# Performance work log

Hardware: AMD Instinct MI355X
Metric: run time of the kernel (lower is better)

Reference implementation:

```python
import jax, jax.numpy as jnp
import numpy as np

N_NODES = 100000
N_EDGES = 600000
N_GRAPHS = 8
D_IN = 256
H = 128
N_CONV = 2  # layers [128,128,128] -> first_h + 2 GINConvs
BN_EPS = 1e-5


def _bn_eval(x, p):
    # p: [4, H] rows = (gamma, beta, running_mean, running_var); eval-mode BatchNorm1d
    g, b, m, v = p[0], p[1], p[2], p[3]
    return (x - m) * jax.lax.rsqrt(v + BN_EPS) * g + b


def setup_inputs() -> dict:
    key = jax.random.key(0)
    ks = jax.random.split(key, 12)
    x = jax.random.normal(ks[0], (N_NODES, D_IN), dtype=jnp.float32)
    edge_index = jax.random.randint(ks[1], (2, N_EDGES), 0, N_NODES, dtype=jnp.int64 if jax.config.jax_enable_x64 else jnp.int32)
    batch = jnp.sort(jax.random.randint(ks[2], (N_NODES,), 0, N_GRAPHS))
    s = 0.05
    w_first = jax.random.normal(ks[3], (D_IN, H), dtype=jnp.float32) * s
    b_first = jax.random.normal(ks[4], (H,), dtype=jnp.float32) * s

    def bn_params(k):
        k1, k2, k3, k4 = jax.random.split(k, 4)
        gamma = jax.random.uniform(k1, (H,), minval=0.5, maxval=1.5)
        beta = jax.random.normal(k2, (H,)) * 0.1
        mean = jax.random.normal(k3, (H,)) * 0.1
        var = jax.random.uniform(k4, (H,), minval=0.5, maxval=1.5)
        return jnp.stack([gamma, beta, mean, var])  # [4, H]

    bn_first = bn_params(ks[5])
    w_conv = jax.random.normal(ks[6], (N_CONV, H, H), dtype=jnp.float32) * s
    b_conv = jax.random.normal(ks[7], (N_CONV, H), dtype=jnp.float32) * s
    bn_conv = jnp.stack([bn_params(k) for k in jax.random.split(ks[8], N_CONV)])  # [2,4,H]
    w_lin = jax.random.normal(ks[9], (N_CONV + 1, H, 1), dtype=jnp.float32) * s
    b_lin = jax.random.normal(ks[10], (N_CONV + 1, 1), dtype=jnp.float32) * s
    return {"x": x, "edge_index": edge_index, "batch": batch,
            "w_first": w_first, "b_first": b_first, "bn_first": bn_first,
            "w_conv": w_conv, "b_conv": b_conv, "bn_conv": bn_conv,
            "w_lin": w_lin, "b_lin": b_lin}


def reference(x, edge_index, batch, w_first, b_first, bn_first, w_conv, b_conv, bn_conv, w_lin, b_lin):
    src, dst = edge_index[0], edge_index[1]
    # first_h: Linear + BN(eval) + ReLU
    h = jax.nn.relu(_bn_eval(x @ w_first + b_first, bn_first))  # [N, H]

    # layer 0: node-level linear head + global max pool
    node_pred = h @ w_lin[0] + b_lin[0]  # [N, 1]
    wsi_pred = jax.ops.segment_max(node_pred, batch, num_segments=N_GRAPHS)  # [G, 1]

    for l in range(N_CONV):
        # GINConv (eps=0, sum aggregation): nn((1+eps)*x_i + sum_{j->i} x_j)
        agg = jax.ops.segment_sum(h[src], dst, num_segments=N_NODES)  # [N, H]
        h = jax.nn.relu(_bn_eval((h + agg) @ w_conv[l] + b_conv[l], bn_conv[l]))
        np_sub = h @ w_lin[l + 1] + b_lin[l + 1]  # [N, 1]
        node_pred = node_pred + np_sub
        wsi_pred = wsi_pred + jax.ops.segment_max(np_sub, batch, num_segments=N_GRAPHS)
        # dropout p=0.0 -> identity
    return wsi_pred, node_pred
```

## Files before the change

### kernel.cpp

```cpp
#include <hip/hip_runtime.h>
#include <hip/hip_bf16.h>

#define H 128
#define D_IN 256
#define NGRAPH 8

typedef __attribute__((ext_vector_type(8))) short bf16x8;
typedef __attribute__((ext_vector_type(4))) float f32x4;
typedef __attribute__((ext_vector_type(4))) int i32x4;

__device__ __forceinline__ unsigned fenc(float f) {
  unsigned u = __float_as_uint(f);
  return (u & 0x80000000u) ? ~u : (u | 0x80000000u);
}
__device__ __forceinline__ float fdec(unsigned e) {
  unsigned v = (e & 0x80000000u) ? (e & 0x7FFFFFFFu) : ~e;
  return __uint_as_float(v);
}
__device__ __forceinline__ unsigned short f2bf(float f) {
  unsigned u = __float_as_uint(f);
  unsigned r = u + 0x7FFFu + ((u >> 16) & 1u);
  return (unsigned short)(r >> 16);
}

__global__ void init_kernel(int* __restrict__ offsets, unsigned* __restrict__ wsi, int n1) {
  int i = blockIdx.x * blockDim.x + threadIdx.x;
  if (i < n1) offsets[i] = 0;
  if (i < 3 * NGRAPH) wsi[i] = 0u;
}

__global__ void count_kernel(const int* __restrict__ dst, int* __restrict__ offsets, int E) {
  int i = blockIdx.x * blockDim.x + threadIdx.x;
  int stride = gridDim.x * blockDim.x;
  for (int e = i; e < E; e += stride) atomicAdd(&offsets[dst[e]], 1);
}

__global__ void __launch_bounds__(1024)
scan_local(int* __restrict__ data, int* __restrict__ bsum, int n) {
  __shared__ int s[1024];
  int tid = threadIdx.x;
  int i = blockIdx.x * 1024 + tid;
  int v = (i < n) ? data[i] : 0;
  s[tid] = v;
  __syncthreads();
  for (int off = 1; off < 1024; off <<= 1) {
    int t = (tid >= off) ? s[tid - off] : 0;
    __syncthreads();
    s[tid] += t;
    __syncthreads();
  }
  if (i < n) data[i] = s[tid] - v;
  if (tid == 1023) bsum[blockIdx.x] = s[1023];
}

__global__ void __launch_bounds__(128)
scan_bsum(int* __restrict__ bsum, int nb) {
  __shared__ int s[128];
  int tid = threadIdx.x;
  int v = (tid < nb) ? bsum[tid] : 0;
  s[tid] = v;
  __syncthreads();
  for (int off = 1; off < 128; off <<= 1) {
    int t = (tid >= off) ? s[tid - off] : 0;
    __syncthreads();
    s[tid] += t;
    __syncthreads();
  }
  if (tid < nb) bsum[tid] = s[tid] - v;
}

__global__ void __launch_bounds__(1024)
scan_add(int* __restrict__ data, const int* __restrict__ bsum, int* __restrict__ cursor,
         int n, int ncur) {
  int i = blockIdx.x * 1024 + threadIdx.x;
  if (i < n) {
    int v = data[i] + bsum[blockIdx.x];
    data[i] = v;
    if (i < ncur) cursor[i] = v;
  }
}

__global__ void fill_kernel(const int* __restrict__ src, const int* __restrict__ dst,
                            int* __restrict__ cursor, int* __restrict__ esrc, int E) {
  int i = blockIdx.x * blockDim.x + threadIdx.x;
  int stride = gridDim.x * blockDim.x;
  for (int e = i; e < E; e += stride) {
    int d = dst[e];
    int p = atomicAdd(&cursor[d], 1);
    esrc[p] = src[e];
  }
}

__global__ void prep_weights(const float* __restrict__ wf, const float* __restrict__ wcv,
                             unsigned short* __restrict__ wTf, unsigned short* __restrict__ wTc) {
  int i = blockIdx.x * 256 + threadIdx.x;
  if (i < H * D_IN) {
    int n = i >> 8, k = i & 255;
    wTf[i] = f2bf(wf[k * H + n]);
  } else if (i < H * D_IN + 2 * H * H) {
    int j = i - H * D_IN;
    int l = j >> 14, r = j & 16383;
    int n = r >> 7, k = r & 127;
    wTc[j] = f2bf(wcv[l * H * H + k * H + n]);
  }
}

template <int K, bool AF32, bool FIRST>
__global__ void __launch_bounds__(256)
gemm_kernel(const void* __restrict__ Ain, const unsigned short* __restrict__ wT,
            const float* __restrict__ bias, const float* __restrict__ bn,
            const float* __restrict__ wlin, const float* __restrict__ blin, int lidx,
            const int* __restrict__ batch, unsigned short* __restrict__ hout,
            float* __restrict__ node_pred, unsigned* __restrict__ wsi, int N) {
  __shared__ char s_tile[4][2048];
  __shared__ float s_head[128][2];
  __shared__ unsigned s_wsi[NGRAPH];
  const int tid = threadIdx.x;
  const int wid = tid >> 6, lane = tid & 63;
  const int wr = wid >> 1, wc = wid & 1;
  const int g = lane >> 4, l15 = lane & 15;
  if (tid < NGRAPH) s_wsi[tid] = 0u;
  __syncthreads();

  const int row0 = blockIdx.x * 128 + wr * 64;
  f32x4 acc[4][4] = {};

#pragma unroll
  for (int k0 = 0; k0 < K; k0 += 32) {
    bf16x8 af[4];
    if (AF32) {
      const float* A = (const float*)Ain;
#pragma unroll
      for (int m = 0; m < 4; ++m) {
        int r = row0 + m * 16 + l15;
        r = (r < N) ? r : (N - 1);
        const float* p = A + (size_t)r * K + k0 + g * 8;
        float4 u0 = *(const float4*)p;
        float4 u1 = *(const float4*)(p + 4);
        union { unsigned short hh[8]; bf16x8 v; } pk;
        pk.hh[0] = f2bf(u0.x); pk.hh[1] = f2bf(u0.y); pk.hh[2] = f2bf(u0.z); pk.hh[3] = f2bf(u0.w);
        pk.hh[4] = f2bf(u1.x); pk.hh[5] = f2bf(u1.y); pk.hh[6] = f2bf(u1.z); pk.hh[7] = f2bf(u1.w);
        af[m] = pk.v;
      }
    } else {
      const unsigned short* A = (const unsigned short*)Ain;
#pragma unroll
      for (int m = 0; m < 4; ++m) {
        int r = row0 + m * 16 + l15;
        r = (r < N) ? r : (N - 1);
        i32x4 q = *(const i32x4*)(A + (size_t)r * K + k0 + g * 8);
        af[m] = *(bf16x8*)&q;
      }
    }
    bf16x8 bfr[4];
#pragma unroll
    for (int n = 0; n < 4; ++n) {
      int c = wc * 64 + n * 16 + l15;
      bfr[n] = *(const bf16x8*)(wT + (size_t)c * K + k0 + g * 8);
    }
#pragma unroll
    for (int m = 0; m < 4; ++m)
#pragma unroll
      for (int n = 0; n < 4; ++n)
        acc[m][n] = __builtin_amdgcn_mfma_f32_16x16x32_bf16(af[m], bfr[n], acc[m][n], 0, 0, 0);
  }

  float sc[4], sh[4], wl[4];
#pragma unroll
  for (int n = 0; n < 4; ++n) {
    int c = wc * 64 + n * 16 + l15;
    float gam = bn[c], bet = bn[H + c], mu = bn[2 * H + c], va = bn[3 * H + c];
    float rs = rsqrtf(va + 1e-5f);
    sc[n] = gam * rs;
    sh[n] = (bias[c] - mu) * gam * rs + bet;
    wl[n] = wlin[c];
  }

  char* aw = s_tile[wid];
#pragma unroll
  for (int m = 0; m < 4; ++m) {
    float pj[4] = {0.f, 0.f, 0.f, 0.f};
#pragma unroll
    for (int n = 0; n < 4; ++n)
#pragma unroll
      for (int j = 0; j < 4; ++j) {
        float hv = fmaxf(acc[m][n][j] * sc[n] + sh[n], 0.f);
        pj[j] += hv * wl[n];
        *(unsigned short*)(aw + (g * 4 + j) * 128 + (n * 16 + l15) * 2) = f2bf(hv);
      }
#pragma unroll
    for (int j = 0; j < 4; ++j) {
      pj[j] += __shfl_xor(pj[j], 1);
      pj[j] += __shfl_xor(pj[j], 2);
      pj[j] += __shfl_xor(pj[j], 4);
      pj[j] += __shfl_xor(pj[j], 8);
    }
    if (l15 == 0) {
#pragma unroll
      for (int j = 0; j < 4; ++j)
        s_head[wr * 64 + m * 16 + g * 4 + j][wc] = pj[j];
    }
    int grb = row0 + m * 16;
#pragma unroll
    for (int it = 0; it < 2; ++it) {
      int bo = lane * 16 + it * 1024;
      int r16 = bo >> 7, inrow = bo & 127;
      if (grb + r16 < N)
        *(i32x4*)((char*)hout + (size_t)(grb + r16) * 256 + wc * 128 + inrow) =
            *(i32x4*)(aw + bo);
    }
  }
  __syncthreads();
  if (tid < 128) {
    int grh = blockIdx.x * 128 + tid;
    if (grh < N) {
      float np = s_head[tid][0] + s_head[tid][1] + blin[lidx];
      if (FIRST) node_pred[grh] = np; else node_pred[grh] += np;
      atomicMax(&s_wsi[batch[grh]], fenc(np));
    }
  }
  __syncthreads();
  if (tid < NGRAPH && s_wsi[tid] != 0u) atomicMax(&wsi[tid], s_wsi[tid]);
}

__global__ void __launch_bounds__(256)
agg_kernel(const unsigned short* __restrict__ h, const int* __restrict__ offsets,
           const int* __restrict__ esrc, unsigned short* __restrict__ tmp, int n) {
  int node = blockIdx.x * 4 + (threadIdx.x >> 6);
  if (node >= n) return;
  int lane = threadIdx.x & 63;
  const unsigned* hw = (const unsigned*)h;
  size_t base = (size_t)node * (H / 2) + lane;
  unsigned u = hw[base];
  float a0 = __uint_as_float((u & 0xFFFFu) << 16);
  float a1 = __uint_as_float(u & 0xFFFF0000u);
  int s = offsets[node], e = offsets[node + 1];
  int j = s;
  for (; j + 4 <= e; j += 4) {
    int i0 = esrc[j], i1 = esrc[j + 1], i2 = esrc[j + 2], i3 = esrc[j + 3];
    unsigned v0 = hw[(size_t)i0 * (H / 2) + lane];
    unsigned v1 = hw[(size_t)i1 * (H / 2) + lane];
    unsigned v2 = hw[(size_t)i2 * (H / 2) + lane];
    unsigned v3 = hw[(size_t)i3 * (H / 2) + lane];
    a0 += __uint_as_float((v0 & 0xFFFFu) << 16) + __uint_as_float((v1 & 0xFFFFu) << 16) +
          __uint_as_float((v2 & 0xFFFFu) << 16) + __uint_as_float((v3 & 0xFFFFu) << 16);
    a1 += __uint_as_float(v0 & 0xFFFF0000u) + __uint_as_float(v1 & 0xFFFF0000u) +
          __uint_as_float(v2 & 0xFFFF0000u) + __uint_as_float(v3 & 0xFFFF0000u);
  }
  for (; j < e; ++j) {
    unsigned v2 = hw[(size_t)esrc[j] * (H / 2) + lane];
    a0 += __uint_as_float((v2 & 0xFFFFu) << 16);
    a1 += __uint_as_float(v2 & 0xFFFF0000u);
  }
  unsigned r = ((unsigned)f2bf(a1) << 16) | (unsigned)f2bf(a0);
  ((unsigned*)tmp)[base] = r;
}

__global__ void finalize_kernel(const unsigned* __restrict__ wsi, float* __restrict__ out) {
  int g = threadIdx.x;
  if (g < NGRAPH) out[g] = fdec(wsi[g]) + fdec(wsi[NGRAPH + g]) + fdec(wsi[2 * NGRAPH + g]);
}

extern "C" void kernel_launch(void* const* d_in, const int* in_sizes, int n_in,
                              void* d_out, int out_size, void* d_ws, size_t ws_size,
                              hipStream_t stream) {
  const float* x        = (const float*)d_in[0];
  const int*   ei       = (const int*)d_in[1];
  const int*   batch    = (const int*)d_in[2];
  const float* w_first  = (const float*)d_in[3];
  const float* b_first  = (const float*)d_in[4];
  const float* bn_first = (const float*)d_in[5];
  const float* w_conv   = (const float*)d_in[6];
  const float* b_conv   = (const float*)d_in[7];
  const float* bn_conv  = (const float*)d_in[8];
  const float* w_lin    = (const float*)d_in[9];
  const float* b_lin    = (const float*)d_in[10];
  float* out = (float*)d_out;

  const int N = in_sizes[0] / D_IN;
  const int E = in_sizes[1] / 2;
  const int* src = ei;
  const int* dst = ei + E;

  char* ws = (char*)d_ws;
  unsigned short* h   = (unsigned short*)ws;
  unsigned short* tmp = h + (size_t)N * H;
  unsigned short* wTf = tmp + (size_t)N * H;
  unsigned short* wTc = wTf + H * D_IN;
  int* offsets = (int*)(wTc + 2 * H * H);
  int* cursor  = offsets + (N + 1);
  int* esrc    = cursor + N;
  int* bsum    = esrc + E;
  unsigned* wsi = (unsigned*)(bsum + 128);
  float* node_pred = out + NGRAPH;

  const int gemm_grid = (N + 127) / 128;
  const int nscan = N + 1;
  const int nb = (nscan + 1023) / 1024;

  init_kernel<<<(N + 256) / 256, 256, 0, stream>>>(offsets, wsi, N + 1);
  count_kernel<<<1024, 256, 0, stream>>>(dst, offsets, E);
  scan_local<<<nb, 1024, 0, stream>>>(offsets, bsum, nscan);
  scan_bsum<<<1, 128, 0, stream>>>(bsum, nb);
  scan_add<<<nb, 1024, 0, stream>>>(offsets, bsum, cursor, nscan, N);
  fill_kernel<<<1024, 256, 0, stream>>>(src, dst, cursor, esrc, E);
  prep_weights<<<256, 256, 0, stream>>>(w_first, w_conv, wTf, wTc);

  gemm_kernel<D_IN, true, true><<<gemm_grid, 256, 0, stream>>>(
      x, wTf, b_first, bn_first, w_lin, b_lin, 0, batch, h, node_pred, wsi, N);
  for (int l = 0; l < 2; ++l) {
    agg_kernel<<<(N + 3) / 4, 256, 0, stream>>>(h, offsets, esrc, tmp, N);
    gemm_kernel<H, false, false><<<gemm_grid, 256, 0, stream>>>(
        tmp, wTc + (size_t)l * H * H, b_conv + (size_t)l * H, bn_conv + (size_t)l * 4 * H,
        w_lin + (size_t)(l + 1) * H, b_lin, l + 1, batch, h, node_pred,
        wsi + (size_t)(l + 1) * NGRAPH, N);
  }
  finalize_kernel<<<1, 64, 0, stream>>>(wsi, out);
}
```

Before: 280.5 us.

## Stage A tile in swizzled LDS with coalesced loads and pack B per k-slice

The GEMM kernel now loads a 64-row A tile cooperatively with fully coalesced vector loads into XOR-swizzled shared memory, instead of each wave doing strided per-lane row fragment loads. Weights are pre-packed by k-slice so each B fragment read is contiguous. The block tile shrinks from 128 to 64 rows with launch bounds raised to allow two blocks per CU, so the grid doubles. This aims to cut the uncoalesced global traffic on the first layer's fp32 input. In exchange it adds an LDS round trip and a barrier, leaves fewer MFMAs per wave, and makes weight fragment reuse less per block.

```diff
diff --git a/kernel.cpp b/kernel.cpp
--- a/kernel.cpp
+++ b/kernel.cpp
@@ -92,78 +92,99 @@
 }
 
 __global__ void prep_weights(const float* __restrict__ wf, const float* __restrict__ wcv,
-                             unsigned short* __restrict__ wTf, unsigned short* __restrict__ wTc) {
+                             unsigned short* __restrict__ Bf, unsigned short* __restrict__ Bc) {
   int i = blockIdx.x * 256 + threadIdx.x;
-  if (i < H * D_IN) {
-    int n = i >> 8, k = i & 255;
-    wTf[i] = f2bf(wf[k * H + n]);
-  } else if (i < H * D_IN + 2 * H * H) {
-    int j = i - H * D_IN;
-    int l = j >> 14, r = j & 16383;
-    int n = r >> 7, k = r & 127;
-    wTc[j] = f2bf(wcv[l * H * H + k * H + n]);
+  if (i < 32768) {
+    int s = i >> 12, r = i & 4095;
+    int c = r >> 5, r2 = r & 31;
+    int g = r2 >> 3, j = r2 & 7;
+    int k = s * 32 + g * 8 + j;
+    Bf[i] = f2bf(wf[k * H + c]);
+  } else {
+    int i2 = i - 32768;
+    int l = i2 >> 14, r = i2 & 16383;
+    int s = r >> 12, rr = r & 4095;
+    int c = rr >> 5, r2 = rr & 31;
+    int g = r2 >> 3, j = r2 & 7;
+    int k = s * 32 + g * 8 + j;
+    Bc[i2] = f2bf(wcv[l * H * H + k * H + c]);
   }
 }
 
 template <int K, bool AF32, bool FIRST>
-__global__ void __launch_bounds__(256)
-gemm_kernel(const void* __restrict__ Ain, const unsigned short* __restrict__ wT,
+__global__ void __launch_bounds__(256, 2)
+gemm_kernel(const void* __restrict__ Ain, const unsigned short* __restrict__ Bpack,
             const float* __restrict__ bias, const float* __restrict__ bn,
             const float* __restrict__ wlin, const float* __restrict__ blin, int lidx,
             const int* __restrict__ batch, unsigned short* __restrict__ hout,
             float* __restrict__ node_pred, unsigned* __restrict__ wsi, int N) {
-  __shared__ char s_tile[4][2048];
-  __shared__ float s_head[128][2];
+  __shared__ char s_a[64 * K * 2];
+  __shared__ float s_head[64][2];
   __shared__ unsigned s_wsi[NGRAPH];
   const int tid = threadIdx.x;
   const int wid = tid >> 6, lane = tid & 63;
   const int wr = wid >> 1, wc = wid & 1;
   const int g = lane >> 4, l15 = lane & 15;
+  const int row0blk = blockIdx.x * 64;
+  constexpr int RB = K * 2;
   if (tid < NGRAPH) s_wsi[tid] = 0u;
-  __syncthreads();
-
-  const int row0 = blockIdx.x * 128 + wr * 64;
-  f32x4 acc[4][4] = {};
-
-#pragma unroll
-  for (int k0 = 0; k0 < K; k0 += 32) {
-    bf16x8 af[4];
-    if (AF32) {
-      const float* A = (const float*)Ain;
-#pragma unroll
-      for (int m = 0; m < 4; ++m) {
-        int r = row0 + m * 16 + l15;
-        r = (r < N) ? r : (N - 1);
-        const float* p = A + (size_t)r * K + k0 + g * 8;
-        float4 u0 = *(const float4*)p;
-        float4 u1 = *(const float4*)(p + 4);
-        union { unsigned short hh[8]; bf16x8 v; } pk;
-        pk.hh[0] = f2bf(u0.x); pk.hh[1] = f2bf(u0.y); pk.hh[2] = f2bf(u0.z); pk.hh[3] = f2bf(u0.w);
-        pk.hh[4] = f2bf(u1.x); pk.hh[5] = f2bf(u1.y); pk.hh[6] = f2bf(u1.z); pk.hh[7] = f2bf(u1.w);
-        af[m] = pk.v;
-      }
-    } else {
-      const unsigned short* A = (const unsigned short*)Ain;
-#pragma unroll
-      for (int m = 0; m < 4; ++m) {
-        int r = row0 + m * 16 + l15;
-        r = (r < N) ? r : (N - 1);
-        i32x4 q = *(const i32x4*)(A + (size_t)r * K + k0 + g * 8);
-        af[m] = *(bf16x8*)&q;
-      }
-    }
+
+  if (AF32) {
+    const float* A = (const float*)Ain;
+#pragma unroll
+    for (int it = 0; it < 16; ++it) {
+      int flat = (it * 256 + tid) * 4;
+      int lr = flat >> 8;
+      int col = flat & 255;
+      int grow = row0blk + lr;
+      grow = (grow < N) ? grow : (N - 1);
+      float4 u = *(const float4*)(A + (size_t)grow * K + col);
+      union { unsigned short hh[4]; uint2 d; } pk;
+      pk.hh[0] = f2bf(u.x); pk.hh[1] = f2bf(u.y);
+      pk.hh[2] = f2bf(u.z); pk.hh[3] = f2bf(u.w);
+      int addr = lr * RB + col * 2;
+      *(uint2*)(s_a + (addr ^ ((lr & 7) << 4))) = pk.d;
+    }
+  } else {
+    const char* A = (const char*)Ain;
+#pragma unroll
+    for (int it = 0; it < 4; ++it) {
+      int unit = it * 256 + tid;
+      int lr = unit >> 4;
+      int cb = (unit & 15) * 16;
+      int grow = row0blk + lr;
+      grow = (grow < N) ? grow : (N - 1);
+      i32x4 q = *(const i32x4*)(A + (size_t)grow * RB + cb);
+      int addr = lr * RB + cb;
+      *(i32x4*)(s_a + (addr ^ ((lr & 7) << 4))) = q;
+    }
+  }
+  __syncthreads();
+
+  f32x4 acc[2][4] = {};
+  const int lrow0 = wr * 32;
+#pragma unroll
+  for (int s = 0; s < K / 32; ++s) {
     bf16x8 bfr[4];
 #pragma unroll
     for (int n = 0; n < 4; ++n) {
       int c = wc * 64 + n * 16 + l15;
-      bfr[n] = *(const bf16x8*)(wT + (size_t)c * K + k0 + g * 8);
-    }
-#pragma unroll
-    for (int m = 0; m < 4; ++m)
+      bfr[n] = *(const bf16x8*)(Bpack + s * 4096 + c * 32 + g * 8);
+    }
+    bf16x8 af[2];
+#pragma unroll
+    for (int m = 0; m < 2; ++m) {
+      int lr = lrow0 + m * 16 + l15;
+      int addr = lr * RB + s * 64 + g * 16;
+      af[m] = *(const bf16x8*)(s_a + (addr ^ ((lr & 7) << 4)));
+    }
+#pragma unroll
+    for (int m = 0; m < 2; ++m)
 #pragma unroll
       for (int n = 0; n < 4; ++n)
         acc[m][n] = __builtin_amdgcn_mfma_f32_16x16x32_bf16(af[m], bfr[n], acc[m][n], 0, 0, 0);
   }
+  __syncthreads();
 
   float sc[4], sh[4], wl[4];
 #pragma unroll
@@ -176,9 +197,9 @@
     wl[n] = wlin[c];
   }
 
-  char* aw = s_tile[wid];
-#pragma unroll
-  for (int m = 0; m < 4; ++m) {
+  char* aw = s_a + wid * 2048;
+#pragma unroll
+  for (int m = 0; m < 2; ++m) {
     float pj[4] = {0.f, 0.f, 0.f, 0.f};
 #pragma unroll
     for (int n = 0; n < 4; ++n)
@@ -198,9 +219,9 @@
     if (l15 == 0) {
 #pragma unroll
       for (int j = 0; j < 4; ++j)
-        s_head[wr * 64 + m * 16 + g * 4 + j][wc] = pj[j];
-    }
-    int grb = row0 + m * 16;
+        s_head[wr * 32 + m * 16 + g * 4 + j][wc] = pj[j];
+    }
+    int grb = row0blk + wr * 32 + m * 16;
 #pragma unroll
     for (int it = 0; it < 2; ++it) {
       int bo = lane * 16 + it * 1024;
@@ -211,8 +232,8 @@
     }
   }
   __syncthreads();
-  if (tid < 128) {
-    int grh = blockIdx.x * 128 + tid;
+  if (tid < 64) {
+    int grh = row0blk + tid;
     if (grh < N) {
       float np = s_head[tid][0] + s_head[tid][1] + blin[lidx];
       if (FIRST) node_pred[grh] = np; else node_pred[grh] += np;
@@ -294,7 +315,7 @@
   unsigned* wsi = (unsigned*)(bsum + 128);
   float* node_pred = out + NGRAPH;
 
-  const int gemm_grid = (N + 127) / 128;
+  const int gemm_grid = (N + 63) / 64;
   const int nscan = N + 1;
   const int nb = (nscan + 1023) / 1024;
 
@@ -311,7 +332,7 @@
   for (int l = 0; l < 2; ++l) {
     agg_kernel<<<(N + 3) / 4, 256, 0, stream>>>(h, offsets, esrc, tmp, N);
     gemm_kernel<H, false, false><<<gemm_grid, 256, 0, stream>>>(
-        tmp, wTc + (size_t)l * H * H, b_conv + (size_t)l * H, bn_conv + (size_t)l * 4 * H,
+        tmp, wTc + (size_t)l * 16384, b_conv + (size_t)l * H, bn_conv + (size_t)l * 4 * H,
         w_lin + (size_t)(l + 1) * H, b_lin, l + 1, batch, h, node_pred,
         wsi + (size_t)(l + 1) * NGRAPH, N);
   }
```

After: 260.0 us. -7.3%, faster.
